# Performance work log

Hardware: AMD Instinct MI355X
Metric: run time of the kernel (lower is better)

## Reference

```python
import jax, jax.numpy as jnp
import numpy as np

FEAT_DIM = 2048
HIDDEN = 1024
ATTN_DIM = 512
BATCH = 128
NPOS = 196


def setup_inputs() -> dict:
    key = jax.random.key(0)
    ks = jax.random.split(key, 8)
    # Linear layers use kaiming-uniform-ish init; plain scaled normal is fine for a numeric baseline.
    def lin(k, fan_in, fan_out):
        k1, k2 = jax.random.split(k)
        bound = 1.0 / np.sqrt(fan_in)
        W = jax.random.uniform(k1, (fan_out, fan_in), jnp.float32, -bound, bound)
        b = jax.random.uniform(k2, (fan_out,), jnp.float32, -bound, bound)
        return W, b
    We, be = lin(ks[0], FEAT_DIM, ATTN_DIM)
    Wd, bd = lin(ks[1], HIDDEN, ATTN_DIM)
    Wf, bf = lin(ks[2], ATTN_DIM, 1)
    encoder_out = jax.random.normal(ks[3], (BATCH, NPOS, FEAT_DIM), jnp.float32)
    hidden = jax.random.normal(ks[4], (BATCH, HIDDEN), jnp.float32)
    return {
        "encoder_out": encoder_out,
        "hidden": hidden,
        "We": We, "be": be,
        "Wd": Wd, "bd": bd,
        "Wf": Wf, "bf": bf,
    }


def reference(encoder_out, hidden, We, be, Wd, bd, Wf, bf):
    # enc: [B, P, A]; dec: [B, 1, A]
    enc = jnp.einsum('bpf,af->bpa', encoder_out, We) + be
    dec = (jnp.einsum('bh,ah->ba', hidden, Wd) + bd)[:, None, :]
    scores = jnp.tanh(enc + dec)
    # full_attn: [A] -> scalar per position; Wf has shape [1, A]
    scores = jnp.einsum('bpa,a->bp', scores, Wf[0]) + bf[0]
    alpha = jax.nn.softmax(scores, axis=1)  # [B, P]
    context = jnp.einsum('bpf,bp->bf', encoder_out, alpha)  # [B, F]
    return context, alpha
```

## Files before the change

kernel.cpp:

```cpp
#include <hip/hip_runtime.h>
#include <hip/hip_bf16.h>

typedef __bf16 bf16x8 __attribute__((ext_vector_type(8)));
typedef __bf16 bf16x4 __attribute__((ext_vector_type(4)));
typedef float f32x4 __attribute__((ext_vector_type(4)));

#define FEAT 2048
#define HID  1024
#define AD   512
#define NB   128
#define NP   196
#define MROWS (NB * NP)
#define BM 128
#define BN 128
#define BK 64
#define NSTEP (FEAT / BK)
#define NBLK (MROWS / BM * 4)

__global__ __launch_bounds__(256) void pack_we_k(const float* __restrict__ We,
                                                 __bf16* __restrict__ Bp) {
    int t = blockIdx.x * 256 + threadIdx.x;
    int a  = t >> 8;
    int f0 = (t & 255) << 3;
    const float4* src = reinterpret_cast<const float4*>(We + ((size_t)a << 11) + f0);
    float4 x0 = src[0], x1 = src[1];
    int nt = a >> 4, r = a & 15;
    int kt = f0 >> 5, g = (f0 >> 3) & 3;
    size_t off = (((size_t)(kt * 32 + nt) * 64) + (r + (g << 4))) << 3;
    union { __bf16 h[8]; bf16x8 v; } u;
    u.h[0] = (__bf16)x0.x; u.h[1] = (__bf16)x0.y; u.h[2] = (__bf16)x0.z; u.h[3] = (__bf16)x0.w;
    u.h[4] = (__bf16)x1.x; u.h[5] = (__bf16)x1.y; u.h[6] = (__bf16)x1.z; u.h[7] = (__bf16)x1.w;
    *reinterpret_cast<bf16x8*>(Bp + off) = u.v;
}

__global__ __launch_bounds__(256) void dec_k(const float* __restrict__ hidden,
                                             const float* __restrict__ Wd,
                                             const float* __restrict__ bd,
                                             const float* __restrict__ be,
                                             float* __restrict__ decb) {
    __shared__ float w[8][1028];
    const int tid = threadIdx.x;
    const int n0 = blockIdx.x << 3;
    const float4* wsrc = reinterpret_cast<const float4*>(Wd + ((size_t)n0 << 10));
    #pragma unroll
    for (int i = 0; i < 8; ++i)
        *reinterpret_cast<float4*>(&w[i][tid << 2]) = wsrc[(i << 8) + tid];
    __syncthreads();
    const int nl = tid & 7, b0 = tid >> 3;
    float acc[4] = {0.f, 0.f, 0.f, 0.f};
    const float4* wp = reinterpret_cast<const float4*>(&w[nl][0]);
    #pragma unroll 2
    for (int k4 = 0; k4 < 256; ++k4) {
        float4 wv = wp[k4];
        #pragma unroll
        for (int i = 0; i < 4; ++i) {
            const float4 h = reinterpret_cast<const float4*>(
                hidden + ((size_t)(b0 + (i << 5)) << 10))[k4];
            acc[i] = fmaf(wv.x, h.x, acc[i]);
            acc[i] = fmaf(wv.y, h.y, acc[i]);
            acc[i] = fmaf(wv.z, h.z, acc[i]);
            acc[i] = fmaf(wv.w, h.w, acc[i]);
        }
    }
    const float bias = bd[n0 + nl] + be[n0 + nl];
    #pragma unroll
    for (int i = 0; i < 4; ++i)
        decb[(size_t)(b0 + (i << 5)) * AD + n0 + nl] = acc[i] + bias;
}

__device__ __forceinline__ void load_a(const float* g, float4 r[8]) {
    #pragma unroll
    for (int i = 0; i < 8; ++i)
        r[i] = *reinterpret_cast<const float4*>(g + (size_t)(i * 16) * FEAT);
}

__device__ __forceinline__ void write_a(char* base, int srow, int schk, const float4 r[8]) {
    #pragma unroll
    for (int i = 0; i < 8; ++i) {
        const int rr = srow + 16 * i;
        union { __bf16 h[4]; bf16x4 v; } p;
        p.h[0] = (__bf16)r[i].x; p.h[1] = (__bf16)r[i].y;
        p.h[2] = (__bf16)r[i].z; p.h[3] = (__bf16)r[i].w;
        *reinterpret_cast<bf16x4*>(base + rr * 128 + ((schk * 8) ^ ((rr & 7) << 4))) = p.v;
    }
}

__device__ __forceinline__ void load_b(const __bf16* bs, bf16x8 f[8]) {
    #pragma unroll
    for (int kt2 = 0; kt2 < 2; ++kt2)
        #pragma unroll
        for (int j = 0; j < 4; ++j)
            f[kt2 * 4 + j] = *reinterpret_cast<const bf16x8*>(bs + kt2 * 16384 + j * 512);
}

__device__ __forceinline__ void mfma_step(const char* buf, const bf16x8 f[8],
                                          int wm, int lr, int lg, int rswz,
                                          f32x4 acc[4][4]) {
    #pragma unroll
    for (int kt2 = 0; kt2 < 2; ++kt2) {
        #pragma unroll
        for (int mt = 0; mt < 4; ++mt) {
            const int R = wm * 64 + mt * 16 + lr;
            bf16x8 a = *reinterpret_cast<const bf16x8*>(
                buf + R * 128 + ((kt2 * 64 + lg * 16) ^ rswz));
            acc[mt][0] = __builtin_amdgcn_mfma_f32_16x16x32_bf16(a, f[kt2*4+0], acc[mt][0], 0, 0, 0);
            acc[mt][1] = __builtin_amdgcn_mfma_f32_16x16x32_bf16(a, f[kt2*4+1], acc[mt][1], 0, 0, 0);
            acc[mt][2] = __builtin_amdgcn_mfma_f32_16x16x32_bf16(a, f[kt2*4+2], acc[mt][2], 0, 0, 0);
            acc[mt][3] = __builtin_amdgcn_mfma_f32_16x16x32_bf16(a, f[kt2*4+3], acc[mt][3], 0, 0, 0);
        }
    }
}

__global__ __launch_bounds__(256, 2) void enc_score_k(
        const float* __restrict__ X, const __bf16* __restrict__ Bp,
        const float* __restrict__ decb, const float* __restrict__ Wf,
        float* __restrict__ spart) {
    __shared__ char Asm0[BM * BK * 2];
    __shared__ char Asm1[BM * BK * 2];
    __shared__ float swave[2][BM];
    const int tid  = threadIdx.x;
    const int wave = tid >> 6, lane = tid & 63;
    const int lr = lane & 15, lg = lane >> 4;
    const int wm = wave >> 1, wn = wave & 1;
    const int vbid = (blockIdx.x & 7) * 98 + (blockIdx.x >> 3);
    const int rt = vbid >> 2, nq = vbid & 3;
    const int row0 = rt * BM;
    const int ncol0 = nq * BN + wn * 64;

    f32x4 acc[4][4];
    #pragma unroll
    for (int mt = 0; mt < 4; ++mt) {
        #pragma unroll
        for (int j = 0; j < 4; ++j) {
            const int row = wm * 64 + mt * 16 + lg * 4 + j;
            const int b = (unsigned)(row0 + row) / 196u;
            const float* dp = decb + (size_t)b * AD + ncol0 + lr;
            #pragma unroll
            for (int nt = 0; nt < 4; ++nt) acc[mt][nt][j] = dp[nt * 16];
        }
    }

    const int srow = tid >> 4;
    const int schk = tid & 15;
    const float* gA = X + (size_t)(row0 + srow) * FEAT + schk * 4;
    const int rswz = (lr & 7) << 4;
    const __bf16* Bq = Bp + ((size_t)(nq * 8 + wn * 4) << 9) + (lane << 3);

    float4 rAa[8], rAb[8];
    bf16x8 bfrA[8], bfrB[8];

    load_a(gA, rAa);
    load_a(gA + BK, rAb);
    load_b(Bq, bfrA);
    write_a(Asm0, srow, schk, rAa);
    asm volatile("s_waitcnt lgkmcnt(0)" ::: "memory");
    __builtin_amdgcn_sched_barrier(0);
    __builtin_amdgcn_s_barrier();

    #pragma unroll 1
    for (int t2 = 0; t2 < NSTEP; t2 += 2) {
        load_b(Bq + (size_t)(t2 + 1) * 32768, bfrB);
        if (t2 + 2 < NSTEP) load_a(gA + (size_t)(t2 + 2) * BK, rAa);
        __builtin_amdgcn_sched_barrier(0);
        mfma_step(Asm0, bfrA, wm, lr, lg, rswz, acc);
        __builtin_amdgcn_sched_barrier(0);
        write_a(Asm1, srow, schk, rAb);
        asm volatile("s_waitcnt lgkmcnt(0)" ::: "memory");
        __builtin_amdgcn_sched_barrier(0);
        __builtin_amdgcn_s_barrier();
        if (t2 + 2 < NSTEP) load_b(Bq + (size_t)(t2 + 2) * 32768, bfrA);
        if (t2 + 3 < NSTEP) load_a(gA + (size_t)(t2 + 3) * BK, rAb);
        __builtin_amdgcn_sched_barrier(0);
        mfma_step(Asm1, bfrB, wm, lr, lg, rswz, acc);
        if (t2 + 2 < NSTEP) {
            __builtin_amdgcn_sched_barrier(0);
            write_a(Asm0, srow, schk, rAa);
            asm volatile("s_waitcnt lgkmcnt(0)" ::: "memory");
            __builtin_amdgcn_sched_barrier(0);
            __builtin_amdgcn_s_barrier();
        }
    }

    float wf[4];
    #pragma unroll
    for (int nt = 0; nt < 4; ++nt) wf[nt] = Wf[ncol0 + nt * 16 + lr];
    #pragma unroll
    for (int mt = 0; mt < 4; ++mt) {
        #pragma unroll
        for (int j = 0; j < 4; ++j) {
            float s = 0.f;
            #pragma unroll
            for (int nt = 0; nt < 4; ++nt) {
                float x = acc[mt][nt][j];
                float e = __expf(2.0f * x);
                float t = 1.0f - 2.0f / (e + 1.0f);
                s = fmaf(t, wf[nt], s);
            }
            s += __shfl_xor(s, 1); s += __shfl_xor(s, 2);
            s += __shfl_xor(s, 4); s += __shfl_xor(s, 8);
            if (lr == 0) swave[wn][wm * 64 + mt * 16 + lg * 4 + j] = s;
        }
    }
    __syncthreads();
    if (tid < BM)
        spart[(size_t)nq * MROWS + row0 + tid] = swave[0][tid] + swave[1][tid];
}

__global__ __launch_bounds__(64) void softmax_k(const float* __restrict__ spart,
                                                float* __restrict__ alpha) {
    const int b = blockIdx.x, lane = threadIdx.x;
    float v[4], e[4];
    float m = -3.0e38f;
    #pragma unroll
    for (int i = 0; i < 4; ++i) {
        int p = i * 64 + lane;
        if (p < NP) {
            int idx = b * NP + p;
            v[i] = spart[idx] + spart[MROWS + idx] + spart[2 * MROWS + idx]
                 + spart[3 * MROWS + idx];
        } else v[i] = -3.0e38f;
        m = fmaxf(m, v[i]);
    }
    #pragma unroll
    for (int o = 1; o < 64; o <<= 1) m = fmaxf(m, __shfl_xor(m, o));
    float s = 0.f;
    #pragma unroll
    for (int i = 0; i < 4; ++i) {
        int p = i * 64 + lane;
        e[i] = (p < NP) ? __expf(v[i] - m) : 0.f;
        s += e[i];
    }
    #pragma unroll
    for (int o = 1; o < 64; o <<= 1) s += __shfl_xor(s, o);
    const float inv = 1.0f / s;
    #pragma unroll
    for (int i = 0; i < 4; ++i) {
        int p = i * 64 + lane;
        if (p < NP) alpha[b * NP + p] = e[i] * inv;
    }
}

__global__ __launch_bounds__(128) void context_k(const float* __restrict__ X,
                                                 const float* __restrict__ alpha,
                                                 float* __restrict__ ctx) {
    __shared__ float al[NP];
    const int bid = blockIdx.x;
    const int b = 127 - (bid >> 2);
    const int chunk = bid & 3;
    const int tid = threadIdx.x;
    for (int i = tid; i < NP; i += 128) al[i] = alpha[b * NP + i];
    __syncthreads();
    const float4* Xp = reinterpret_cast<const float4*>(X + (size_t)b * NP * FEAT)
                       + chunk * 128 + tid;
    float4 a0 = {0,0,0,0}, a1 = {0,0,0,0};
    #pragma unroll 4
    for (int p = 0; p < NP; p += 2) {
        const float w0 = al[p], w1 = al[p + 1];
        const float4 x0 = Xp[(size_t)p * 512];
        const float4 x1 = Xp[(size_t)(p + 1) * 512];
        a0.x = fmaf(w0, x0.x, a0.x); a0.y = fmaf(w0, x0.y, a0.y);
        a0.z = fmaf(w0, x0.z, a0.z); a0.w = fmaf(w0, x0.w, a0.w);
        a1.x = fmaf(w1, x1.x, a1.x); a1.y = fmaf(w1, x1.y, a1.y);
        a1.z = fmaf(w1, x1.z, a1.z); a1.w = fmaf(w1, x1.w, a1.w);
    }
    float4 rr; rr.x = a0.x + a1.x; rr.y = a0.y + a1.y; rr.z = a0.z + a1.z; rr.w = a0.w + a1.w;
    *reinterpret_cast<float4*>(ctx + (size_t)b * FEAT + chunk * 512 + tid * 4) = rr;
}

extern "C" void kernel_launch(void* const* d_in, const int* in_sizes, int n_in,
                              void* d_out, int out_size, void* d_ws, size_t ws_size,
                              hipStream_t stream) {
    const float* enc    = (const float*)d_in[0];
    const float* hidden = (const float*)d_in[1];
    const float* We     = (const float*)d_in[2];
    const float* be     = (const float*)d_in[3];
    const float* Wd     = (const float*)d_in[4];
    const float* bd     = (const float*)d_in[5];
    const float* Wf     = (const float*)d_in[6];

    float* out   = (float*)d_out;
    float* ctx   = out;
    float* alpha = out + NB * FEAT;

    char* ws = (char*)d_ws;
    __bf16* Bp    = (__bf16*)ws;
    float*  decb  = (float*)(ws + (2u << 20));
    float*  spart = (float*)(ws + (2u << 20) + (256u << 10));

    pack_we_k  <<<dim3(512), dim3(256), 0, stream>>>(We, Bp);
    dec_k      <<<dim3(64),  dim3(256), 0, stream>>>(hidden, Wd, bd, be, decb);
    enc_score_k<<<dim3(NBLK), dim3(256), 0, stream>>>(enc, Bp, decb, Wf, spart);
    softmax_k  <<<dim3(NB),  dim3(64),  0, stream>>>(spart, alpha);
    context_k  <<<dim3(512), dim3(128), 0, stream>>>(enc, alpha, ctx);
}
```

Baseline: 175.7 us.

## Give each wave a private LDS A tile to drop block barriers

```diff
diff --git a/kernel.cpp b/kernel.cpp
--- a/kernel.cpp
+++ b/kernel.cpp
@@ -68,20 +68,21 @@
         decb[(size_t)(b0 + (i << 5)) * AD + n0 + nl] = acc[i] + bias;
 }
 
-__device__ __forceinline__ void load_a(const float* g, float4 r[8]) {
-    #pragma unroll
-    for (int i = 0; i < 8; ++i)
-        r[i] = *reinterpret_cast<const float4*>(g + (size_t)(i * 16) * FEAT);
-}
-
-__device__ __forceinline__ void write_a(char* base, int srow, int schk, const float4 r[8]) {
-    #pragma unroll
-    for (int i = 0; i < 8; ++i) {
-        const int rr = srow + 16 * i;
+__device__ __forceinline__ void load_a16(const float* g, float4 r[16]) {
+    #pragma unroll
+    for (int i = 0; i < 16; ++i)
+        r[i] = *reinterpret_cast<const float4*>(g + (size_t)(i * 4) * FEAT);
+}
+
+__device__ __forceinline__ void write_a16(char* base, int lrow, int scol,
+                                          const float4 r[16]) {
+    #pragma unroll
+    for (int i = 0; i < 16; ++i) {
+        const int rr = lrow + 4 * i;
         union { __bf16 h[4]; bf16x4 v; } p;
         p.h[0] = (__bf16)r[i].x; p.h[1] = (__bf16)r[i].y;
         p.h[2] = (__bf16)r[i].z; p.h[3] = (__bf16)r[i].w;
-        *reinterpret_cast<bf16x4*>(base + rr * 128 + ((schk * 8) ^ ((rr & 7) << 4))) = p.v;
+        *reinterpret_cast<bf16x4*>(base + rr * 128 + (scol ^ ((rr & 7) << 4))) = p.v;
     }
 }
 
@@ -94,13 +95,12 @@
 }
 
 __device__ __forceinline__ void mfma_step(const char* buf, const bf16x8 f[8],
-                                          int wm, int lr, int lg, int rswz,
-                                          f32x4 acc[4][4]) {
+                                          int lr, int lg, int rswz, f32x4 acc[4][4]) {
     #pragma unroll
     for (int kt2 = 0; kt2 < 2; ++kt2) {
         #pragma unroll
         for (int mt = 0; mt < 4; ++mt) {
-            const int R = wm * 64 + mt * 16 + lr;
+            const int R = mt * 16 + lr;
             bf16x8 a = *reinterpret_cast<const bf16x8*>(
                 buf + R * 128 + ((kt2 * 64 + lg * 16) ^ rswz));
             acc[mt][0] = __builtin_amdgcn_mfma_f32_16x16x32_bf16(a, f[kt2*4+0], acc[mt][0], 0, 0, 0);
@@ -115,8 +115,8 @@
         const float* __restrict__ X, const __bf16* __restrict__ Bp,
         const float* __restrict__ decb, const float* __restrict__ Wf,
         float* __restrict__ spart) {
-    __shared__ char Asm0[BM * BK * 2];
-    __shared__ char Asm1[BM * BK * 2];
+    __shared__ char Asm0[4][8192];
+    __shared__ char Asm1[4][8192];
     __shared__ float swave[2][BM];
     const int tid  = threadIdx.x;
     const int wave = tid >> 6, lane = tid & 63;
@@ -140,45 +140,34 @@
         }
     }
 
-    const int srow = tid >> 4;
-    const int schk = tid & 15;
-    const float* gA = X + (size_t)(row0 + srow) * FEAT + schk * 4;
+    char* wb0 = Asm0[wave];
+    char* wb1 = Asm1[wave];
+    const int lrow = lane >> 4;
+    const int scol = (lane & 15) * 8;
+    const float* gA = X + (size_t)(row0 + wm * 64 + lrow) * FEAT + (lane & 15) * 4;
     const int rswz = (lr & 7) << 4;
     const __bf16* Bq = Bp + ((size_t)(nq * 8 + wn * 4) << 9) + (lane << 3);
 
-    float4 rAa[8], rAb[8];
+    float4 rA[16];
     bf16x8 bfrA[8], bfrB[8];
 
-    load_a(gA, rAa);
-    load_a(gA + BK, rAb);
+    load_a16(gA, rA);
     load_b(Bq, bfrA);
-    write_a(Asm0, srow, schk, rAa);
-    asm volatile("s_waitcnt lgkmcnt(0)" ::: "memory");
-    __builtin_amdgcn_sched_barrier(0);
-    __builtin_amdgcn_s_barrier();
+    write_a16(wb0, lrow, scol, rA);
+    load_a16(gA + BK, rA);
+    load_b(Bq + 32768, bfrB);
 
     #pragma unroll 1
     for (int t2 = 0; t2 < NSTEP; t2 += 2) {
-        load_b(Bq + (size_t)(t2 + 1) * 32768, bfrB);
-        if (t2 + 2 < NSTEP) load_a(gA + (size_t)(t2 + 2) * BK, rAa);
-        __builtin_amdgcn_sched_barrier(0);
-        mfma_step(Asm0, bfrA, wm, lr, lg, rswz, acc);
-        __builtin_amdgcn_sched_barrier(0);
-        write_a(Asm1, srow, schk, rAb);
-        asm volatile("s_waitcnt lgkmcnt(0)" ::: "memory");
-        __builtin_amdgcn_sched_barrier(0);
-        __builtin_amdgcn_s_barrier();
-        if (t2 + 2 < NSTEP) load_b(Bq + (size_t)(t2 + 2) * 32768, bfrA);
-        if (t2 + 3 < NSTEP) load_a(gA + (size_t)(t2 + 3) * BK, rAb);
-        __builtin_amdgcn_sched_barrier(0);
-        mfma_step(Asm1, bfrB, wm, lr, lg, rswz, acc);
-        if (t2 + 2 < NSTEP) {
-            __builtin_amdgcn_sched_barrier(0);
-            write_a(Asm0, srow, schk, rAa);
-            asm volatile("s_waitcnt lgkmcnt(0)" ::: "memory");
-            __builtin_amdgcn_sched_barrier(0);
-            __builtin_amdgcn_s_barrier();
-        }
+        const bool more = (t2 + 2 < NSTEP);
+        write_a16(wb1, lrow, scol, rA);
+        if (more) load_a16(gA + (size_t)(t2 + 2) * BK, rA);
+        mfma_step(wb0, bfrA, lr, lg, rswz, acc);
+        if (more) load_b(Bq + (size_t)(t2 + 2) * 32768, bfrA);
+        if (more) write_a16(wb0, lrow, scol, rA);
+        if (t2 + 3 < NSTEP) load_a16(gA + (size_t)(t2 + 3) * BK, rA);
+        mfma_step(wb1, bfrB, lr, lg, rswz, acc);
+        if (t2 + 3 < NSTEP) load_b(Bq + (size_t)(t2 + 3) * 32768, bfrB);
     }
 
     float wf[4];
```

New measurement: 203.6 us. +15.9%, slower.
